# Kernel optimization log

Hardware: AMD Instinct MI355X
Metric: run time of the kernel (lower is better)

## Reference

```python
import jax, jax.numpy as jnp
import numpy as np

B, T, D, TY = 64, 512, 96, 512
H, DK = 4, 32            # num_heads, embed_dim_per_head
E = H * DK               # embed_dim = 128
P = 2                    # function='L' -> 2 coefficients
L, HID = 64, 128         # latent_dim, hidden_dim


def setup_inputs() -> dict:
    key = jax.random.key(0)
    ks = jax.random.split(key, 16)
    inp = {
        "timesteps": jax.random.uniform(ks[0], (B, T), jnp.float32),
        "X": jax.random.normal(ks[1], (B, T, D), jnp.float32),
        "M": jax.random.randint(ks[2], (B, T, D), 0, 2).astype(jnp.float32),
        "y_time_steps": jax.random.uniform(ks[3], (B, TY), jnp.float32),
        # time_embedding: Linear(1, E)
        "te_w": jax.random.normal(ks[4], (E,), jnp.float32),
        "te_b": jax.random.normal(ks[5], (E,), jnp.float32) * 0.1,
        # learned query [1, P, E]
        "query": jax.random.normal(ks[6], (1, P, E), jnp.float32),
        # query_map / key_map: Linear(E, E), stored [in, out]
        "q_w": jax.random.normal(ks[7], (E, E), jnp.float32) / np.sqrt(E),
        "q_b": jax.random.normal(ks[8], (E,), jnp.float32) * 0.1,
        "k_w": jax.random.normal(ks[9], (E, E), jnp.float32) / np.sqrt(E),
        "k_b": jax.random.normal(ks[10], (E,), jnp.float32) * 0.1,
        # attn shared out: Linear(2D*H, L)
        "ow": jax.random.normal(ks[11], (2 * D * H, L), jnp.float32) / np.sqrt(2 * D * H),
        "ob": jnp.zeros((L,), jnp.float32),
        # decoder MLP: Linear(L,HID)+ReLU+Linear(HID,D)
        "w1": jax.random.normal(ks[12], (L, HID), jnp.float32) / np.sqrt(L),
        "b1": jnp.zeros((HID,), jnp.float32),
        "w2": jax.random.normal(ks[13], (HID, D), jnp.float32) / np.sqrt(HID),
        "b2": jnp.zeros((D,), jnp.float32),
    }
    return inp


def _fld_forward(timesteps, X, M, y_time_steps, te_w, te_b, query,
                 q_w, q_b, k_w, k_b, ow, ob, w1, b1, w2, b2):
    b, t, d = X.shape
    # time embedding: Linear(1,E), sin applied to indices i % H == 0
    emb = timesteps[..., None] * te_w + te_b               # [B,T,E]
    sin_idx = (jnp.arange(E) % H) == 0
    emb = jnp.where(sin_idx, jnp.sin(emb), emb)

    X_cat = jnp.concatenate([X, M], axis=-1)               # [B,T,2D]
    M_cat = jnp.concatenate([M, M], axis=-1)               # [B,T,2D]

    q = query @ q_w + q_b                                   # [1,P,E]
    k = emb @ k_w + k_b                                     # [B,T,E]
    q = q.reshape(1, P, H, DK).transpose(0, 2, 1, 3)        # [1,H,P,dk]
    k = k.reshape(b, t, H, DK).transpose(0, 2, 1, 3)        # [B,H,T,dk]

    scores = jnp.einsum('xhpd,bhtd->bhpt', q, k) / np.sqrt(DK)  # [B,H,P,T]
    # broadcast over value feature dim, mask per-feature, softmax over T
    logits = jnp.where(M_cat[:, None, None, :, :] == 0, -jnp.inf,
                       scores[..., None])                   # [B,H,P,T,2D]
    p = jax.nn.softmax(logits, axis=-2)
    xa = jnp.einsum('bhptf,btf->bhpf', p, X_cat)            # [B,H,P,2D]
    xa = xa.transpose(0, 2, 1, 3).reshape(b, P, H * 2 * d)  # [B,P,H*2D]
    coeffs = xa @ ow + ob                                   # [B,P,L]

    # function 'L': linear in y_time_steps
    x = coeffs[:, 0][:, None, :] + y_time_steps[:, :, None] * coeffs[:, 1][:, None, :]
    h1 = jax.nn.relu(x @ w1 + b1)
    return h1 @ w2 + b2                                     # [B,TY,D]


def reference(timesteps, X, M, y_time_steps, te_w, te_b, query,
              q_w, q_b, k_w, k_b, ow, ob, w1, b1, w2, b2):
    return _fld_forward(timesteps, X, M, y_time_steps, te_w, te_b, query,
                        q_w, q_b, k_w, k_b, ow, ob, w1, b1, w2, b2)
```

## Files before the change

### kernel.cpp

```cpp
#include <hip/hip_runtime.h>
#include <math.h>

#define B_   64
#define T_   512
#define D_   96
#define TY_  512
#define H_   4
#define DK_  32
#define E_   128
#define P_   2
#define L_   64
#define HID_ 128

#define WS_OB2P  1024
#define WS_PN    2048
#define WS_PD    395264

#define TS_  194

__global__ __launch_bounds__(256) void kphase1(
    const float* __restrict__ tsteps, const float* __restrict__ te_w,
    const float* __restrict__ te_b,   const float* __restrict__ X,
    const float* __restrict__ M,      const float* __restrict__ query,
    const float* __restrict__ q_w,    const float* __restrict__ q_b,
    const float* __restrict__ k_w,    const float* __restrict__ k_b,
    const float* __restrict__ ow,     float* __restrict__ ws)
{
    const int bi = blockIdx.x, tid = threadIdx.x;
    const int c = bi & 7, b = bi >> 3;

    __shared__ float qm[P_ * E_];
    __shared__ float w2q_s[E_ * 8];
    __shared__ float tw_s[E_], tb_s[E_], bq_s[8];
    __shared__ float w_sB[64][8];
    __shared__ float red[96 * 17];
    __shared__ float obp2[4][64];

    {
        int p = tid >> 7, ep = tid & 127;
        float acc = q_b[ep];
        #pragma unroll 8
        for (int e = 0; e < E_; ++e)
            acc += query[p * E_ + e] * q_w[e * E_ + ep];
        qm[p * E_ + ep] = acc;
    }
    if (tid < E_) { tw_s[tid] = te_w[tid]; tb_s[tid] = te_b[tid]; }
    __syncthreads();
    const float rs = 0.17677669529663687f;
    #pragma unroll
    for (int i = 0; i < 4; ++i) {
        int idx = tid + i * 256;
        int e = idx >> 3, hp = idx & 7, h = hp >> 1, p = hp & 1;
        float acc = 0.f;
        #pragma unroll
        for (int dk = 0; dk < DK_; ++dk)
            acc += k_w[e * E_ + h * DK_ + dk] * qm[p * E_ + h * DK_ + dk];
        w2q_s[idx] = acc * rs;
    }
    if (tid < 8) {
        int hp = tid, h = hp >> 1, p = hp & 1;
        float acc = 0.f;
        #pragma unroll
        for (int dk = 0; dk < DK_; ++dk)
            acc += k_b[h * DK_ + dk] * qm[p * E_ + h * DK_ + dk];
        bq_s[hp] = acc * rs;
    }
    __syncthreads();

    {
        const int t = tid & 63, hpg = tid >> 6, hp0 = hpg * 2;
        const float tv = tsteps[b * T_ + c * 64 + t];
        float a0 = 0.f, a1 = 0.f;
        #pragma unroll 4
        for (int e = 0; e < E_; ++e) {
            float v = tv * tw_s[e] + tb_s[e];
            if ((e & 3) == 0) v = __sinf(v);
            float2 w = *(const float2*)&w2q_s[e * 8 + hp0];
            a0 += v * w.x;
            a1 += v * w.y;
        }
        float e0 = __expf(a0 + bq_s[hp0]);
        float e1 = __expf(a1 + bq_s[hp0 + 1]);
        *(float2*)&w_sB[t][hp0] = make_float2(e0, e1);
    }
    __syncthreads();

    const int fid = tid & 127, slice = tid >> 7;
    float num[8] = {0.f, 0.f, 0.f, 0.f, 0.f, 0.f, 0.f, 0.f};
    float den[8] = {0.f, 0.f, 0.f, 0.f, 0.f, 0.f, 0.f, 0.f};
    if (fid < 96) {
        #pragma unroll 4
        for (int i = 0; i < 32; ++i) {
            int tl = slice + 2 * i;
            size_t base = ((size_t)(b * T_ + c * 64 + tl)) * D_ + fid;
            float m = M[base], x = X[base];
            float mx = m * x;
            float4 wa = *(const float4*)&w_sB[tl][0];
            float4 wb = *(const float4*)&w_sB[tl][4];
            float wv[8];
            *(float4*)&wv[0] = wa; *(float4*)&wv[4] = wb;
            #pragma unroll
            for (int hp = 0; hp < 8; ++hp) {
                num[hp] += wv[hp] * mx;
                den[hp] += wv[hp] * m;
            }
        }
    }
    __syncthreads();
    if (slice == 1 && fid < 96) {
        #pragma unroll
        for (int hp = 0; hp < 8; ++hp) {
            red[fid * 17 + hp]     = num[hp];
            red[fid * 17 + 8 + hp] = den[hp];
        }
    }
    __syncthreads();
    if (slice == 0 && fid < 96) {
        float* pN = ws + WS_PN + ((size_t)((b * 8 + c) * 8)) * 96;
        float* pD = ws + WS_PD + ((size_t)((b * 8 + c) * 8)) * 96;
        #pragma unroll
        for (int hp = 0; hp < 8; ++hp) {
            pN[hp * 96 + fid] = num[hp] + red[fid * 17 + hp];
            pD[hp * 96 + fid] = den[hp] + red[fid * 17 + 8 + hp];
        }
    }

    if (b == 0) {
        int sub = tid >> 6, l = tid & 63;
        float acc = 0.f;
        #pragma unroll
        for (int k = 0; k < 12; ++k) {
            int hj = c * 48 + sub * 12 + k;
            int h = hj / 96, j = hj - h * 96;
            acc += ow[(size_t)(h * 2 * D_ + D_ + j) * L_ + l];
        }
        obp2[sub][l] = acc;
        __syncthreads();
        if (sub == 0)
            ws[WS_OB2P + c * 64 + l] = obp2[0][l] + obp2[1][l]
                                     + obp2[2][l] + obp2[3][l];
    }
}

__global__ __launch_bounds__(1024) void kfuse2(
    const float* __restrict__ ow, const float* __restrict__ ob,
    const float* __restrict__ w1, const float* __restrict__ b1,
    const float* __restrict__ yts, const float* __restrict__ w2,
    const float* __restrict__ b2, const float* __restrict__ ws,
    float* __restrict__ out)
{
    __shared__ float w2_s[HID_ * D_];
    union Tail {
        float tab[129 * TS_];
        struct {
            float xa[768];
            float cfp[4][2][64];
            float abp[2][2][128];
        } e;
    };
    __shared__ Tail u;
    __shared__ float cf_s[2][64];
    __shared__ float ab0_s[HID_], ab1_s[HID_];
    __shared__ float t_s[HID_], u_s[HID_], vt_s[HID_], c0_s[HID_];
    __shared__ float ts_s[HID_];
    __shared__ int   sidx_s[HID_];
    __shared__ float base0_s[96], base1_s[96];

    const int bi = blockIdx.x, tid = threadIdx.x;
    const int b = bi >> 2, bq = bi & 3;

    {
        const float4* src = (const float4*)w2;
        float4* dst = (float4*)w2_s;
        #pragma unroll
        for (int i = 0; i < 3; ++i) dst[tid + i * 1024] = src[tid + i * 1024];
    }

    if (tid < 768) {
        int hp = tid / 96, f = tid - hp * 96;
        float n = 0.f, d = 0.f;
        #pragma unroll
        for (int cc = 0; cc < 8; ++cc) {
            n += ws[WS_PN + ((size_t)((b * 8 + cc) * 8 + hp)) * 96 + f];
            d += ws[WS_PD + ((size_t)((b * 8 + cc) * 8 + hp)) * 96 + f];
        }
        u.e.xa[tid] = n / d;
    }
    __syncthreads();

    if (tid < 512) {
        int h = tid >> 7, p = (tid >> 6) & 1, l = tid & 63;
        const float* xr = u.e.xa + (h * 2 + p) * 96;
        const float* owr = ow + (size_t)(h * 2 * D_) * L_ + l;
        float acc = 0.f;
        #pragma unroll 8
        for (int f = 0; f < 96; ++f)
            acc += xr[f] * owr[(size_t)f * L_];
        u.e.cfp[h][p][l] = acc;
    }
    __syncthreads();

    if (tid < 128) {
        int p = tid >> 6, l = tid & 63;
        float v = u.e.cfp[0][p][l] + u.e.cfp[1][p][l] + u.e.cfp[2][p][l]
                + u.e.cfp[3][p][l] + ob[l];
        #pragma unroll
        for (int g = 0; g < 8; ++g) v += ws[WS_OB2P + g * 64 + l];
        cf_s[p][l] = v;
    }
    __syncthreads();

    if (tid < 256) {
        int s = tid >> 7, j = tid & 127;
        float a0 = 0.f, a1 = 0.f;
        #pragma unroll 4
        for (int li = 0; li < 32; ++li) {
            int l = s * 32 + li;
            float wv = w1[l * HID_ + j];
            a0 += cf_s[0][l] * wv;
            a1 += cf_s[1][l] * wv;
        }
        u.e.abp[s][0][j] = a0;
        u.e.abp[s][1][j] = a1;
    }
    __syncthreads();

    if (tid < 128) {
        ab0_s[tid] = u.e.abp[0][0][tid] + u.e.abp[1][0][tid] + b1[tid];
    } else if (tid < 256) {
        int j = tid - 128;
        ab1_s[j] = u.e.abp[0][1][j] + u.e.abp[1][1][j];
    }
    __syncthreads();

    if (tid < 128) {
        float a0 = ab0_s[tid], a1 = ab1_s[tid];
        float t, uu, vt, c0;
        if (a1 > 0.f)      { t = -a0 / a1;  uu =  a1; vt = -a0; c0 = 0.f; }
        else if (a1 < 0.f) { t = -a0 / a1;  uu = -a1; vt =  a0; c0 = 0.f; }
        else               { t = INFINITY;  uu = 0.f; vt = 0.f; c0 = fabsf(a0); }
        t_s[tid] = t; u_s[tid] = uu; vt_s[tid] = vt; c0_s[tid] = c0;
    }
    __syncthreads();

    if (tid < 128) {
        float tj = t_s[tid];
        int r = 0;
        #pragma unroll 8
        for (int k = 0; k < 128; ++k) {
            float tk = t_s[k];
            r += (tk < tj) || (tk == tj && k < tid);
        }
        sidx_s[r] = tid;
    }
    __syncthreads();

    if (tid < 96) {
        float g0 = 0.f, g1 = 0.f, ut = 0.f, vta = 0.f, cc2 = 0.f;
        #pragma unroll 4
        for (int j = 0; j < 128; ++j) {
            float wv = w2_s[j * 96 + tid];
            g0  += ab0_s[j] * wv;
            g1  += ab1_s[j] * wv;
            ut  += u_s[j]  * wv;
            vta += vt_s[j] * wv;
            cc2 += c0_s[j] * wv;
        }
        base0_s[tid] = 0.5f * (g0 + cc2 + vta) + b2[tid];
        base1_s[tid] = 0.5f * (g1 - ut);
    } else if (tid >= 128 && tid < 256) {
        int k = tid - 128;
        ts_s[k] = t_s[sidx_s[k]];
    }
    __syncthreads();

    if (tid < 96) {
        float cur0 = base0_s[tid], cur1 = base1_s[tid];
        u.tab[tid] = cur0;
        u.tab[96 + tid] = cur1;
        #pragma unroll 4
        for (int k = 0; k < 128; ++k) {
            int j = sidx_s[k];
            float wv = w2_s[j * 96 + tid];
            cur0 -= vt_s[j] * wv;
            cur1 += u_s[j] * wv;
            u.tab[(k + 1) * TS_ + tid]      = cur0;
            u.tab[(k + 1) * TS_ + 96 + tid] = cur1;
        }
    }
    __syncthreads();

    {
        const int pos = tid >> 3, oct = tid & 7;
        const int gpos = bq * 128 + pos;
        const float y = yts[b * TY_ + gpos];

        int lo = 0, hi = 128;
        #pragma unroll
        for (int s = 0; s < 7; ++s) {
            int mid = (lo + hi) >> 1;
            if (ts_s[mid] < y) lo = mid + 1; else hi = mid;
        }

        const float* R = u.tab + lo * TS_ + oct * 12;
        float vout[12];
        #pragma unroll
        for (int q = 0; q < 6; ++q) {
            float2 r0 = *(const float2*)(R + 2 * q);
            float2 r1 = *(const float2*)(R + 96 + 2 * q);
            vout[2 * q]     = r0.x + y * r1.x;
            vout[2 * q + 1] = r0.y + y * r1.y;
        }
        float* op = out + ((size_t)(b * TY_ + gpos)) * D_ + oct * 12;
        #pragma unroll
        for (int s = 0; s < 3; ++s)
            *(float4*)(op + 4 * s) = make_float4(vout[4 * s], vout[4 * s + 1],
                                                 vout[4 * s + 2], vout[4 * s + 3]);
    }
}

extern "C" void kernel_launch(void* const* d_in, const int* in_sizes, int n_in,
                              void* d_out, int out_size, void* d_ws, size_t ws_size,
                              hipStream_t stream)
{
    const float* timesteps = (const float*)d_in[0];
    const float* X         = (const float*)d_in[1];
    const float* M         = (const float*)d_in[2];
    const float* yts       = (const float*)d_in[3];
    const float* te_w      = (const float*)d_in[4];
    const float* te_b      = (const float*)d_in[5];
    const float* query     = (const float*)d_in[6];
    const float* q_w       = (const float*)d_in[7];
    const float* q_b       = (const float*)d_in[8];
    const float* k_w       = (const float*)d_in[9];
    const float* k_b       = (const float*)d_in[10];
    const float* ow        = (const float*)d_in[11];
    const float* ob        = (const float*)d_in[12];
    const float* w1        = (const float*)d_in[13];
    const float* b1        = (const float*)d_in[14];
    const float* w2        = (const float*)d_in[15];
    const float* b2        = (const float*)d_in[16];
    float* out = (float*)d_out;
    float* ws  = (float*)d_ws;

    kphase1<<<512, 256, 0, stream>>>(timesteps, te_w, te_b, X, M, query,
                                     q_w, q_b, k_w, k_b, ow, ws);
    kfuse2<<<4 * B_, 1024, 0, stream>>>(ow, ob, w1, b1, yts, w2, b2, ws, out);
}
```

Baseline: 148.1 us.

## Fuse attention pooling and decoder into a single kernel per batch quarter

Merges the two launches into one kernel where each block recomputes query/key projections, timestep weights and the full masked softmax pooling over all timesteps for its batch, then proceeds to the decoder. This removes the global workspace writes/reads, the inter-kernel dependency and the constant ow-sum precompute. In exchange each batch's attention reduction is done redundantly by four blocks, quadrupling X/M reads and per-block compute.

```diff
diff --git a/kernel.cpp b/kernel.cpp
--- a/kernel.cpp
+++ b/kernel.cpp
@@ -12,153 +12,39 @@
 #define L_   64
 #define HID_ 128
 
-#define WS_OB2P  1024
-#define WS_PN    2048
-#define WS_PD    395264
-
 #define TS_  194
 
-__global__ __launch_bounds__(256) void kphase1(
+__global__ __launch_bounds__(1024) void kone(
     const float* __restrict__ tsteps, const float* __restrict__ te_w,
     const float* __restrict__ te_b,   const float* __restrict__ X,
     const float* __restrict__ M,      const float* __restrict__ query,
     const float* __restrict__ q_w,    const float* __restrict__ q_b,
     const float* __restrict__ k_w,    const float* __restrict__ k_b,
-    const float* __restrict__ ow,     float* __restrict__ ws)
-{
-    const int bi = blockIdx.x, tid = threadIdx.x;
-    const int c = bi & 7, b = bi >> 3;
-
-    __shared__ float qm[P_ * E_];
-    __shared__ float w2q_s[E_ * 8];
-    __shared__ float tw_s[E_], tb_s[E_], bq_s[8];
-    __shared__ float w_sB[64][8];
-    __shared__ float red[96 * 17];
-    __shared__ float obp2[4][64];
-
-    {
-        int p = tid >> 7, ep = tid & 127;
-        float acc = q_b[ep];
-        #pragma unroll 8
-        for (int e = 0; e < E_; ++e)
-            acc += query[p * E_ + e] * q_w[e * E_ + ep];
-        qm[p * E_ + ep] = acc;
-    }
-    if (tid < E_) { tw_s[tid] = te_w[tid]; tb_s[tid] = te_b[tid]; }
-    __syncthreads();
-    const float rs = 0.17677669529663687f;
-    #pragma unroll
-    for (int i = 0; i < 4; ++i) {
-        int idx = tid + i * 256;
-        int e = idx >> 3, hp = idx & 7, h = hp >> 1, p = hp & 1;
-        float acc = 0.f;
-        #pragma unroll
-        for (int dk = 0; dk < DK_; ++dk)
-            acc += k_w[e * E_ + h * DK_ + dk] * qm[p * E_ + h * DK_ + dk];
-        w2q_s[idx] = acc * rs;
-    }
-    if (tid < 8) {
-        int hp = tid, h = hp >> 1, p = hp & 1;
-        float acc = 0.f;
-        #pragma unroll
-        for (int dk = 0; dk < DK_; ++dk)
-            acc += k_b[h * DK_ + dk] * qm[p * E_ + h * DK_ + dk];
-        bq_s[hp] = acc * rs;
-    }
-    __syncthreads();
-
-    {
-        const int t = tid & 63, hpg = tid >> 6, hp0 = hpg * 2;
-        const float tv = tsteps[b * T_ + c * 64 + t];
-        float a0 = 0.f, a1 = 0.f;
-        #pragma unroll 4
-        for (int e = 0; e < E_; ++e) {
-            float v = tv * tw_s[e] + tb_s[e];
-            if ((e & 3) == 0) v = __sinf(v);
-            float2 w = *(const float2*)&w2q_s[e * 8 + hp0];
-            a0 += v * w.x;
-            a1 += v * w.y;
-        }
-        float e0 = __expf(a0 + bq_s[hp0]);
-        float e1 = __expf(a1 + bq_s[hp0 + 1]);
-        *(float2*)&w_sB[t][hp0] = make_float2(e0, e1);
-    }
-    __syncthreads();
-
-    const int fid = tid & 127, slice = tid >> 7;
-    float num[8] = {0.f, 0.f, 0.f, 0.f, 0.f, 0.f, 0.f, 0.f};
-    float den[8] = {0.f, 0.f, 0.f, 0.f, 0.f, 0.f, 0.f, 0.f};
-    if (fid < 96) {
-        #pragma unroll 4
-        for (int i = 0; i < 32; ++i) {
-            int tl = slice + 2 * i;
-            size_t base = ((size_t)(b * T_ + c * 64 + tl)) * D_ + fid;
-            float m = M[base], x = X[base];
-            float mx = m * x;
-            float4 wa = *(const float4*)&w_sB[tl][0];
-            float4 wb = *(const float4*)&w_sB[tl][4];
-            float wv[8];
-            *(float4*)&wv[0] = wa; *(float4*)&wv[4] = wb;
-            #pragma unroll
-            for (int hp = 0; hp < 8; ++hp) {
-                num[hp] += wv[hp] * mx;
-                den[hp] += wv[hp] * m;
-            }
-        }
-    }
-    __syncthreads();
-    if (slice == 1 && fid < 96) {
-        #pragma unroll
-        for (int hp = 0; hp < 8; ++hp) {
-            red[fid * 17 + hp]     = num[hp];
-            red[fid * 17 + 8 + hp] = den[hp];
-        }
-    }
-    __syncthreads();
-    if (slice == 0 && fid < 96) {
-        float* pN = ws + WS_PN + ((size_t)((b * 8 + c) * 8)) * 96;
-        float* pD = ws + WS_PD + ((size_t)((b * 8 + c) * 8)) * 96;
-        #pragma unroll
-        for (int hp = 0; hp < 8; ++hp) {
-            pN[hp * 96 + fid] = num[hp] + red[fid * 17 + hp];
-            pD[hp * 96 + fid] = den[hp] + red[fid * 17 + 8 + hp];
-        }
-    }
-
-    if (b == 0) {
-        int sub = tid >> 6, l = tid & 63;
-        float acc = 0.f;
-        #pragma unroll
-        for (int k = 0; k < 12; ++k) {
-            int hj = c * 48 + sub * 12 + k;
-            int h = hj / 96, j = hj - h * 96;
-            acc += ow[(size_t)(h * 2 * D_ + D_ + j) * L_ + l];
-        }
-        obp2[sub][l] = acc;
-        __syncthreads();
-        if (sub == 0)
-            ws[WS_OB2P + c * 64 + l] = obp2[0][l] + obp2[1][l]
-                                     + obp2[2][l] + obp2[3][l];
-    }
-}
-
-__global__ __launch_bounds__(1024) void kfuse2(
-    const float* __restrict__ ow, const float* __restrict__ ob,
-    const float* __restrict__ w1, const float* __restrict__ b1,
-    const float* __restrict__ yts, const float* __restrict__ w2,
-    const float* __restrict__ b2, const float* __restrict__ ws,
-    float* __restrict__ out)
+    const float* __restrict__ ow,     const float* __restrict__ ob,
+    const float* __restrict__ w1,     const float* __restrict__ b1,
+    const float* __restrict__ yts,    const float* __restrict__ w2,
+    const float* __restrict__ b2,     float* __restrict__ out)
 {
     __shared__ float w2_s[HID_ * D_];
-    union Tail {
+    union U {
         float tab[129 * TS_];
         struct {
-            float xa[768];
-            float cfp[4][2][64];
-            float abp[2][2][128];
-        } e;
+            union {
+                float w_sB[512][8];
+                struct {
+                    float xa[768];
+                    float cfp[4][2][64];
+                    float abp[2][2][128];
+                } c;
+            } f;
+            float redN[8][8][96];
+            float redD[8][8][96];
+            float qm[P_ * E_];
+            float w2q[E_ * 8];
+            float tw[E_], tb[E_], bq[8];
+        } p;
     };
-    __shared__ Tail u;
+    __shared__ U u;
     __shared__ float cf_s[2][64];
     __shared__ float ab0_s[HID_], ab1_s[HID_];
     __shared__ float t_s[HID_], u_s[HID_], vt_s[HID_], c0_s[HID_];
@@ -167,7 +53,7 @@
     __shared__ float base0_s[96], base1_s[96];
 
     const int bi = blockIdx.x, tid = threadIdx.x;
-    const int b = bi >> 2, bq = bi & 3;
+    const int b = bi >> 2, bq4 = bi & 3;
 
     {
         const float4* src = (const float4*)w2;
@@ -175,38 +61,119 @@
         #pragma unroll
         for (int i = 0; i < 3; ++i) dst[tid + i * 1024] = src[tid + i * 1024];
     }
+    if (tid < E_) { u.p.tw[tid] = te_w[tid]; u.p.tb[tid] = te_b[tid]; }
+
+    if (tid < 256) {
+        int p = tid >> 7, ep = tid & 127;
+        float acc = q_b[ep];
+        #pragma unroll 8
+        for (int e = 0; e < E_; ++e)
+            acc += query[p * E_ + e] * q_w[e * E_ + ep];
+        u.p.qm[p * E_ + ep] = acc;
+    }
+    __syncthreads();
+
+    const float rs = 0.17677669529663687f;
+    {
+        int e = tid >> 3, hp = tid & 7, h = hp >> 1, p = hp & 1;
+        float acc = 0.f;
+        #pragma unroll
+        for (int dk = 0; dk < DK_; ++dk)
+            acc += k_w[e * E_ + h * DK_ + dk] * u.p.qm[p * E_ + h * DK_ + dk];
+        u.p.w2q[tid] = acc * rs;
+    }
+    if (tid < 8) {
+        int hp = tid, h = hp >> 1, p = hp & 1;
+        float acc = 0.f;
+        #pragma unroll
+        for (int dk = 0; dk < DK_; ++dk)
+            acc += k_b[h * DK_ + dk] * u.p.qm[p * E_ + h * DK_ + dk];
+        u.p.bq[hp] = acc * rs;
+    }
+    __syncthreads();
+
+    {
+        const int t = tid >> 1, g = tid & 1, hp0 = g * 4;
+        const float tv = tsteps[b * T_ + t];
+        float a0 = 0.f, a1 = 0.f, a2 = 0.f, a3 = 0.f;
+        #pragma unroll 4
+        for (int e = 0; e < E_; ++e) {
+            float v = tv * u.p.tw[e] + u.p.tb[e];
+            if ((e & 3) == 0) v = __sinf(v);
+            float4 w = *(const float4*)&u.p.w2q[e * 8 + hp0];
+            a0 += v * w.x; a1 += v * w.y; a2 += v * w.z; a3 += v * w.w;
+        }
+        float4 eo;
+        eo.x = __expf(a0 + u.p.bq[hp0]);
+        eo.y = __expf(a1 + u.p.bq[hp0 + 1]);
+        eo.z = __expf(a2 + u.p.bq[hp0 + 2]);
+        eo.w = __expf(a3 + u.p.bq[hp0 + 3]);
+        *(float4*)&u.p.f.w_sB[t][hp0] = eo;
+    }
+    __syncthreads();
+
+    {
+        const int fid = tid & 127, slice = tid >> 7;
+        float num[8] = {0.f,0.f,0.f,0.f,0.f,0.f,0.f,0.f};
+        float den[8] = {0.f,0.f,0.f,0.f,0.f,0.f,0.f,0.f};
+        if (fid < 96) {
+            #pragma unroll 4
+            for (int i = 0; i < 64; ++i) {
+                int tl = slice + 8 * i;
+                size_t base = ((size_t)(b * T_ + tl)) * D_ + fid;
+                float m = M[base], x = X[base];
+                float mx = m * x;
+                float4 wa = *(const float4*)&u.p.f.w_sB[tl][0];
+                float4 wb = *(const float4*)&u.p.f.w_sB[tl][4];
+                float wv[8];
+                *(float4*)&wv[0] = wa; *(float4*)&wv[4] = wb;
+                #pragma unroll
+                for (int hp = 0; hp < 8; ++hp) {
+                    num[hp] += wv[hp] * mx;
+                    den[hp] += wv[hp] * m;
+                }
+            }
+            #pragma unroll
+            for (int hp = 0; hp < 8; ++hp) {
+                u.p.redN[slice][hp][fid] = num[hp];
+                u.p.redD[slice][hp][fid] = den[hp];
+            }
+        }
+    }
+    __syncthreads();
 
     if (tid < 768) {
         int hp = tid / 96, f = tid - hp * 96;
         float n = 0.f, d = 0.f;
         #pragma unroll
-        for (int cc = 0; cc < 8; ++cc) {
-            n += ws[WS_PN + ((size_t)((b * 8 + cc) * 8 + hp)) * 96 + f];
-            d += ws[WS_PD + ((size_t)((b * 8 + cc) * 8 + hp)) * 96 + f];
-        }
-        u.e.xa[tid] = n / d;
+        for (int s = 0; s < 8; ++s) {
+            n += u.p.redN[s][hp][f];
+            d += u.p.redD[s][hp][f];
+        }
+        u.p.f.c.xa[tid] = n / d;
     }
     __syncthreads();
 
     if (tid < 512) {
         int h = tid >> 7, p = (tid >> 6) & 1, l = tid & 63;
-        const float* xr = u.e.xa + (h * 2 + p) * 96;
-        const float* owr = ow + (size_t)(h * 2 * D_) * L_ + l;
-        float acc = 0.f;
-        #pragma unroll 8
+        const float* xr   = u.p.f.c.xa + (h * 2 + p) * 96;
+        const float* owr  = ow + (size_t)(h * 2 * D_) * L_ + l;
+        const float* owr2 = ow + (size_t)(h * 2 * D_ + D_) * L_ + l;
+        float acc = 0.f, acc2 = 0.f;
+        #pragma unroll 4
         for (int f = 0; f < 96; ++f)
             acc += xr[f] * owr[(size_t)f * L_];
-        u.e.cfp[h][p][l] = acc;
+        #pragma unroll 4
+        for (int j = 0; j < 96; ++j)
+            acc2 += owr2[(size_t)j * L_];
+        u.p.f.c.cfp[h][p][l] = acc + acc2;
     }
     __syncthreads();
 
     if (tid < 128) {
         int p = tid >> 6, l = tid & 63;
-        float v = u.e.cfp[0][p][l] + u.e.cfp[1][p][l] + u.e.cfp[2][p][l]
-                + u.e.cfp[3][p][l] + ob[l];
-        #pragma unroll
-        for (int g = 0; g < 8; ++g) v += ws[WS_OB2P + g * 64 + l];
-        cf_s[p][l] = v;
+        cf_s[p][l] = u.p.f.c.cfp[0][p][l] + u.p.f.c.cfp[1][p][l]
+                   + u.p.f.c.cfp[2][p][l] + u.p.f.c.cfp[3][p][l] + ob[l];
     }
     __syncthreads();
 
@@ -220,16 +187,16 @@
             a0 += cf_s[0][l] * wv;
             a1 += cf_s[1][l] * wv;
         }
-        u.e.abp[s][0][j] = a0;
-        u.e.abp[s][1][j] = a1;
+        u.p.f.c.abp[s][0][j] = a0;
+        u.p.f.c.abp[s][1][j] = a1;
     }
     __syncthreads();
 
     if (tid < 128) {
-        ab0_s[tid] = u.e.abp[0][0][tid] + u.e.abp[1][0][tid] + b1[tid];
+        ab0_s[tid] = u.p.f.c.abp[0][0][tid] + u.p.f.c.abp[1][0][tid] + b1[tid];
     } else if (tid < 256) {
         int j = tid - 128;
-        ab1_s[j] = u.e.abp[0][1][j] + u.e.abp[1][1][j];
+        ab1_s[j] = u.p.f.c.abp[0][1][j] + u.p.f.c.abp[1][1][j];
     }
     __syncthreads();
 
@@ -292,7 +259,7 @@
 
     {
         const int pos = tid >> 3, oct = tid & 7;
-        const int gpos = bq * 128 + pos;
+        const int gpos = bq4 * 128 + pos;
         const float y = yts[b * TY_ + gpos];
 
         int lo = 0, hi = 128;
@@ -341,9 +308,9 @@
     const float* w2        = (const float*)d_in[15];
     const float* b2        = (const float*)d_in[16];
     float* out = (float*)d_out;
-    float* ws  = (float*)d_ws;
-
-    kphase1<<<512, 256, 0, stream>>>(timesteps, te_w, te_b, X, M, query,
-                                     q_w, q_b, k_w, k_b, ow, ws);
-    kfuse2<<<4 * B_, 1024, 0, stream>>>(ow, ob, w1, b1, yts, w2, b2, ws, out);
+    (void)d_ws; (void)ws_size;
+
+    kone<<<4 * B_, 1024, 0, stream>>>(timesteps, te_w, te_b, X, M, query,
+                                      q_w, q_b, k_w, k_b, ow, ob, w1, b1,
+                                      yts, w2, b2, out);
 }
```

Result: slower. 165.4 us (+11.7%).

## Double phase-1 block size to 512 threads and defer w2 smem store in kfuse2

Applied to the files above, without the earlier changes.

kphase1 now runs 512 threads per block on a 2D grid. Each thread computes one head/query score instead of two, and the time dimension is split four ways with a three-way shared-memory reduction, so more warps are in flight to hide X/M loads. kfuse2 loads w2 into registers up front and writes it to shared memory later, so the global load overlaps the partial-sum reduction. The trade-off is more shared memory and registers per block, plus a larger reduction step.

```diff
diff --git a/kernel.cpp b/kernel.cpp
--- a/kernel.cpp
+++ b/kernel.cpp
@@ -18,7 +18,7 @@
 
 #define TS_  194
 
-__global__ __launch_bounds__(256) void kphase1(
+__global__ __launch_bounds__(512) void kphase1(
     const float* __restrict__ tsteps, const float* __restrict__ te_w,
     const float* __restrict__ te_b,   const float* __restrict__ X,
     const float* __restrict__ M,      const float* __restrict__ query,
@@ -26,30 +26,33 @@
     const float* __restrict__ k_w,    const float* __restrict__ k_b,
     const float* __restrict__ ow,     float* __restrict__ ws)
 {
-    const int bi = blockIdx.x, tid = threadIdx.x;
-    const int c = bi & 7, b = bi >> 3;
+    const int c = blockIdx.x, b = blockIdx.y, tid = threadIdx.x;
 
     __shared__ float qm[P_ * E_];
     __shared__ float w2q_s[E_ * 8];
     __shared__ float tw_s[E_], tb_s[E_], bq_s[8];
-    __shared__ float w_sB[64][8];
-    __shared__ float red[96 * 17];
-    __shared__ float obp2[4][64];
-
-    {
+    __shared__ float wB[8][64];
+    __shared__ float redN[3][8][96];
+    __shared__ float redD[3][8][96];
+    __shared__ float obp2[8][64];
+
+    if (tid < 256) {
         int p = tid >> 7, ep = tid & 127;
         float acc = q_b[ep];
         #pragma unroll 8
         for (int e = 0; e < E_; ++e)
             acc += query[p * E_ + e] * q_w[e * E_ + ep];
         qm[p * E_ + ep] = acc;
-    }
-    if (tid < E_) { tw_s[tid] = te_w[tid]; tb_s[tid] = te_b[tid]; }
+    } else if (tid < 384) {
+        int e = tid - 256;
+        tw_s[e] = te_w[e];
+        tb_s[e] = te_b[e];
+    }
     __syncthreads();
     const float rs = 0.17677669529663687f;
     #pragma unroll
-    for (int i = 0; i < 4; ++i) {
-        int idx = tid + i * 256;
+    for (int i = 0; i < 2; ++i) {
+        int idx = tid + i * 512;
         int e = idx >> 3, hp = idx & 7, h = hp >> 1, p = hp & 1;
         float acc = 0.f;
         #pragma unroll
@@ -68,50 +71,43 @@
     __syncthreads();
 
     {
-        const int t = tid & 63, hpg = tid >> 6, hp0 = hpg * 2;
+        const int t = tid & 63, hp = tid >> 6;
         const float tv = tsteps[b * T_ + c * 64 + t];
-        float a0 = 0.f, a1 = 0.f;
+        float a = 0.f;
         #pragma unroll 4
         for (int e = 0; e < E_; ++e) {
             float v = tv * tw_s[e] + tb_s[e];
             if ((e & 3) == 0) v = __sinf(v);
-            float2 w = *(const float2*)&w2q_s[e * 8 + hp0];
-            a0 += v * w.x;
-            a1 += v * w.y;
-        }
-        float e0 = __expf(a0 + bq_s[hp0]);
-        float e1 = __expf(a1 + bq_s[hp0 + 1]);
-        *(float2*)&w_sB[t][hp0] = make_float2(e0, e1);
+            a += v * w2q_s[e * 8 + hp];
+        }
+        wB[hp][t] = __expf(a + bq_s[hp]);
     }
     __syncthreads();
 
     const int fid = tid & 127, slice = tid >> 7;
-    float num[8] = {0.f, 0.f, 0.f, 0.f, 0.f, 0.f, 0.f, 0.f};
-    float den[8] = {0.f, 0.f, 0.f, 0.f, 0.f, 0.f, 0.f, 0.f};
+    float num[8] = {0.f,0.f,0.f,0.f,0.f,0.f,0.f,0.f};
+    float den[8] = {0.f,0.f,0.f,0.f,0.f,0.f,0.f,0.f};
     if (fid < 96) {
         #pragma unroll 4
-        for (int i = 0; i < 32; ++i) {
-            int tl = slice + 2 * i;
+        for (int i = 0; i < 16; ++i) {
+            int tl = slice + 4 * i;
             size_t base = ((size_t)(b * T_ + c * 64 + tl)) * D_ + fid;
             float m = M[base], x = X[base];
             float mx = m * x;
-            float4 wa = *(const float4*)&w_sB[tl][0];
-            float4 wb = *(const float4*)&w_sB[tl][4];
-            float wv[8];
-            *(float4*)&wv[0] = wa; *(float4*)&wv[4] = wb;
             #pragma unroll
             for (int hp = 0; hp < 8; ++hp) {
-                num[hp] += wv[hp] * mx;
-                den[hp] += wv[hp] * m;
+                float wv = wB[hp][tl];
+                num[hp] += wv * mx;
+                den[hp] += wv * m;
             }
         }
     }
     __syncthreads();
-    if (slice == 1 && fid < 96) {
+    if (slice > 0 && fid < 96) {
         #pragma unroll
         for (int hp = 0; hp < 8; ++hp) {
-            red[fid * 17 + hp]     = num[hp];
-            red[fid * 17 + 8 + hp] = den[hp];
+            redN[slice - 1][hp][fid] = num[hp];
+            redD[slice - 1][hp][fid] = den[hp];
         }
     }
     __syncthreads();
@@ -120,8 +116,10 @@
         float* pD = ws + WS_PD + ((size_t)((b * 8 + c) * 8)) * 96;
         #pragma unroll
         for (int hp = 0; hp < 8; ++hp) {
-            pN[hp * 96 + fid] = num[hp] + red[fid * 17 + hp];
-            pD[hp * 96 + fid] = den[hp] + red[fid * 17 + 8 + hp];
+            pN[hp * 96 + fid] = num[hp] + redN[0][hp][fid]
+                              + redN[1][hp][fid] + redN[2][hp][fid];
+            pD[hp * 96 + fid] = den[hp] + redD[0][hp][fid]
+                              + redD[1][hp][fid] + redD[2][hp][fid];
         }
     }
 
@@ -129,16 +127,19 @@
         int sub = tid >> 6, l = tid & 63;
         float acc = 0.f;
         #pragma unroll
-        for (int k = 0; k < 12; ++k) {
-            int hj = c * 48 + sub * 12 + k;
+        for (int k = 0; k < 6; ++k) {
+            int hj = c * 48 + sub * 6 + k;
             int h = hj / 96, j = hj - h * 96;
             acc += ow[(size_t)(h * 2 * D_ + D_ + j) * L_ + l];
         }
         obp2[sub][l] = acc;
         __syncthreads();
-        if (sub == 0)
-            ws[WS_OB2P + c * 64 + l] = obp2[0][l] + obp2[1][l]
-                                     + obp2[2][l] + obp2[3][l];
+        if (sub == 0) {
+            float v = 0.f;
+            #pragma unroll
+            for (int s = 0; s < 8; ++s) v += obp2[s][l];
+            ws[WS_OB2P + c * 64 + l] = v;
+        }
     }
 }
 
@@ -167,13 +168,13 @@
     __shared__ float base0_s[96], base1_s[96];
 
     const int bi = blockIdx.x, tid = threadIdx.x;
-    const int b = bi >> 2, bq = bi & 3;
-
+    const int b = bi >> 2, bq4 = bi & 3;
+
+    float4 wreg[3];
     {
         const float4* src = (const float4*)w2;
-        float4* dst = (float4*)w2_s;
-        #pragma unroll
-        for (int i = 0; i < 3; ++i) dst[tid + i * 1024] = src[tid + i * 1024];
+        #pragma unroll
+        for (int i = 0; i < 3; ++i) wreg[i] = src[tid + i * 1024];
     }
 
     if (tid < 768) {
@@ -231,6 +232,11 @@
         int j = tid - 128;
         ab1_s[j] = u.e.abp[0][1][j] + u.e.abp[1][1][j];
     }
+    {
+        float4* dst = (float4*)w2_s;
+        #pragma unroll
+        for (int i = 0; i < 3; ++i) dst[tid + i * 1024] = wreg[i];
+    }
     __syncthreads();
 
     if (tid < 128) {
@@ -292,7 +298,7 @@
 
     {
         const int pos = tid >> 3, oct = tid & 7;
-        const int gpos = bq * 128 + pos;
+        const int gpos = bq4 * 128 + pos;
         const float y = yts[b * TY_ + gpos];
 
         int lo = 0, hi = 128;
@@ -343,7 +349,7 @@
     float* out = (float*)d_out;
     float* ws  = (float*)d_ws;
 
-    kphase1<<<512, 256, 0, stream>>>(timesteps, te_w, te_b, X, M, query,
-                                     q_w, q_b, k_w, k_b, ow, ws);
+    kphase1<<<dim3(8, B_), 512, 0, stream>>>(timesteps, te_w, te_b, X, M,
+                                             query, q_w, q_b, k_w, k_b, ow, ws);
     kfuse2<<<4 * B_, 1024, 0, stream>>>(ow, ob, w1, b1, yts, w2, b2, ws, out);
 }
```

Result: slower. 156.1 us (+5.4%).
